# Kernel optimization log

Hardware: AMD Instinct MI355X
Metric: run time of the kernel (lower is better)

## Reference

```python
import jax, jax.numpy as jnp
import numpy as np

N, N_HUB, N_TOP = 1024, 512, 256
D_NODE, D_W, H = 128, 16, 64
E_FULL = N * (N - 1) // 2
E_HUB = N_HUB * (N_HUB - 1) // 2
E_TOP = N_TOP * (N_TOP - 1) // 2
SLOPE = 0.01  # torch F.leaky_relu default negative slope


def leaky(x):
    return jnp.where(x >= 0, x, SLOPE * x)


def gcn_conv(x, src, dst, ew, W, b, n):
    # PyG GCNConv: add self-loops (weight 1), symmetric deg^-1/2 normalization,
    # weighted sum-aggregation at destination nodes.
    loop = jnp.arange(n)
    s = jnp.concatenate([src, loop])
    d = jnp.concatenate([dst, loop])
    w = jnp.concatenate([ew, jnp.ones((n,), ew.dtype)])
    deg = jax.ops.segment_sum(w, d, num_segments=n)
    deg_safe = jnp.where(deg > 0, deg, 1.0)
    dinv = jnp.where(deg > 0, jax.lax.rsqrt(deg_safe), 0.0)
    norm = dinv[s] * w * dinv[d]          # [E + n]
    h = x @ W                              # [n, out]
    msg = h[s] * norm[:, None]             # gather + scale
    return jax.ops.segment_sum(msg, d, num_segments=n) + b


def fusion(node_attr, src, dst, edge_attr, dgW, dgb, gW, gb, cW, cb, adj_sel, edge_mask, n):
    # EdgeNodeFusion forward (dropout_rate = 0 -> dropout is identity)
    ea = leaky(edge_attr @ dgW + dgb)                       # deep-gravity Linear + LeakyReLU
    if edge_mask is not None:
        ea = ea[edge_mask]                                  # gather branch edges [E_b, H]
    sel = ea[adj_sel]                                       # directed edge attrs [E_b, H]
    s2 = jnp.concatenate([src, dst])                        # to_undirected: duplicate both ways
    d2 = jnp.concatenate([dst, src])
    w2 = jnp.concatenate([sel, sel], axis=0).mean(axis=1)   # AdaptiveAvgPool1d(1) over features
    xh = leaky(gcn_conv(node_attr, s2, d2, w2, gW, gb, n))  # [n, out]
    sim = jax.nn.sigmoid(xh @ xh.T)                         # [n, n]
    iu = jnp.triu_indices(n, k=1)
    tri = sim[iu[0], iu[1]]                                 # diag_flatten: strict upper tri, [n(n-1)/2]
    w = tri[:, None] * cW[0] + cb                           # Linear(1 -> H)
    return w * ea + ea, xh


def setup_inputs():
    key = jax.random.key(0)
    ks = jax.random.split(key, 16)
    rng = np.random.default_rng(0)

    def tri_edges(n):
        iu = np.triu_indices(n, k=1)
        return jnp.asarray(np.stack(iu).astype(np.int32))

    def lin(k, fi, fo):
        kw, kb = jax.random.split(k)
        s = 1.0 / np.sqrt(fi)
        return (jax.random.uniform(kw, (fi, fo), jnp.float32, -s, s),
                jax.random.uniform(kb, (fo,), jnp.float32, -s, s))

    inp = {}
    inp['node_hidden_z'] = jax.random.normal(ks[0], (N, D_NODE), jnp.float32)
    inp['weather_x'] = jax.random.normal(ks[1], (N, D_W), jnp.float32)
    inp['hub_weather_x'] = jax.random.normal(ks[2], (N_HUB, D_W), jnp.float32)
    inp['top_weather_x'] = jax.random.normal(ks[3], (N_TOP, D_W), jnp.float32)
    inp['edge_hidden_z'] = jax.random.normal(ks[4], (E_FULL, H), jnp.float32)
    inp['adj_index'] = tri_edges(N)
    inp['hub_adj_index'] = tri_edges(N_HUB)
    inp['top_adj_index'] = tri_edges(N_TOP)
    inp['hub_idx'] = jnp.asarray(np.sort(rng.choice(N, N_HUB, replace=False)).astype(np.int32))
    inp['top_idx'] = jnp.asarray(np.sort(rng.choice(N, N_TOP, replace=False)).astype(np.int32))
    inp['adj_sel_full'] = jnp.arange(E_FULL, dtype=jnp.int32)
    inp['adj_sel_hub'] = jnp.arange(E_HUB, dtype=jnp.int32)
    inp['adj_sel_top'] = jnp.arange(E_TOP, dtype=jnp.int32)
    inp['hub_edge_mask'] = jnp.asarray(np.sort(rng.choice(E_FULL, E_HUB, replace=False)).astype(np.int32))
    inp['top_edge_mask'] = jnp.asarray(np.sort(rng.choice(E_FULL, E_TOP, replace=False)).astype(np.int32))

    D_IN = D_NODE + D_W
    inp['dg_top_W'], inp['dg_top_b'] = lin(ks[5], H, H)
    inp['gcn_top_W'], inp['gcn_top_b'] = lin(ks[6], D_IN, D_NODE)
    inp['cat_top_W'], inp['cat_top_b'] = lin(ks[7], 1, H)
    inp['dg_hub_W'], inp['dg_hub_b'] = lin(ks[8], H, H)
    inp['gcn_hub_W'], inp['gcn_hub_b'] = lin(ks[9], D_IN, H)
    inp['cat_hub_W'], inp['cat_hub_b'] = lin(ks[10], 1, H)
    inp['dg_W'], inp['dg_b'] = lin(ks[11], H, H)
    inp['gcn_W'], inp['gcn_b'] = lin(ks[12], D_IN, H)
    inp['cat_W'], inp['cat_b'] = lin(ks[13], 1, H)
    return inp


def reference(node_hidden_z, weather_x, hub_weather_x, top_weather_x, edge_hidden_z,
              adj_index, hub_adj_index, top_adj_index, hub_idx, top_idx,
              adj_sel_full, adj_sel_hub, adj_sel_top, hub_edge_mask, top_edge_mask,
              dg_top_W, dg_top_b, gcn_top_W, gcn_top_b, cat_top_W, cat_top_b,
              dg_hub_W, dg_hub_b, gcn_hub_W, gcn_hub_b, cat_hub_W, cat_hub_b,
              dg_W, dg_b, gcn_W, gcn_b, cat_W, cat_b):
    # --- top branch ---
    top_x = jnp.concatenate([node_hidden_z[top_idx], top_weather_x], axis=-1)
    top_ea, _ = fusion(top_x, top_adj_index[0], top_adj_index[1], edge_hidden_z,
                       dg_top_W, dg_top_b, gcn_top_W, gcn_top_b, cat_top_W, cat_top_b,
                       adj_sel_top, top_edge_mask, N_TOP)
    top_full = jnp.zeros((E_FULL, H), top_ea.dtype).at[top_edge_mask].set(top_ea)  # edge_unpool
    # --- hub branch ---
    hub_x = jnp.concatenate([node_hidden_z[hub_idx], hub_weather_x], axis=-1)
    hub_ea, _ = fusion(hub_x, hub_adj_index[0], hub_adj_index[1], edge_hidden_z,
                       dg_hub_W, dg_hub_b, gcn_hub_W, gcn_hub_b, cat_hub_W, cat_hub_b,
                       adj_sel_hub, hub_edge_mask, N_HUB)
    hub_full = jnp.zeros((E_FULL, H), hub_ea.dtype).at[hub_edge_mask].set(hub_ea)  # edge_unpool
    # --- full branch ---
    x = jnp.concatenate([node_hidden_z, weather_x], axis=-1)
    full_ea, _ = fusion(x, adj_index[0], adj_index[1], edge_hidden_z,
                        dg_W, dg_b, gcn_W, gcn_b, cat_W, cat_b,
                        adj_sel_full, None, N)
    return jnp.concatenate([top_full, hub_full, full_ea], axis=-1)  # [E_FULL, 3H]


if __name__ == '__main__':
    out = reference(**setup_inputs())
    print(out.shape, out.dtype)
```

## Files before the change

kernel.cpp:

```cpp
#include <hip/hip_runtime.h>
#include <stdint.h>

#define NFULL 1024
#define NHUB  512
#define NTOP  256
#define EFULL 523776
#define EHUB  130816
#define ETOP  32640
#define ETOT  (ETOP + EHUB + EFULL)
#define NTOT  (NTOP + NHUB + NFULL)
#define HOFF_H 32768
#define HOFF_F 65536
#define HTOT   131072
#define SLOPE 0.01f

#define NB_T2 255
#define NB_H2 1022
#define NB_F2 4092

#define TT_T 10
#define TT_H 36
#define TT_F 136

__device__ __forceinline__ int trioff(int i, int n){ return (i * (2 * n - i - 1)) >> 1; }

__global__ void k_init(int* __restrict__ invT, int* __restrict__ invH)
{
  int t = blockIdx.x * 256 + threadIdx.x;
  if (t < EFULL){ invT[t] = -1; invH[t] = -1; }
}

__global__ void k_inv(const int* __restrict__ tmask, const int* __restrict__ hmask,
                      int* __restrict__ invT, int* __restrict__ invH)
{
  int t = blockIdx.x * 256 + threadIdx.x;
  if (t < ETOP) invT[tmask[t]] = t;
  else if (t < ETOP + EHUB) invH[hmask[t - ETOP]] = t - ETOP;
}

__global__ __launch_bounds__(256, 4)
void k_ea_all(const float* __restrict__ ez,
              const int* __restrict__ tmask, const int* __restrict__ hmask,
              const float* __restrict__ Wt, const float* __restrict__ bt,
              const float* __restrict__ Wh, const float* __restrict__ bh,
              const float* __restrict__ Wf, const float* __restrict__ bf,
              float* __restrict__ eat, float* __restrict__ w2_all)
{
  __shared__ float sW[4096];
  __shared__ float sB[64];
  int b = blockIdx.x, tid = threadIdx.x;
  int bloc, w2off; const int* mask; const float* W; const float* bb;
  if (b < NB_T2)               { bloc = b;                 w2off = 0;           mask = tmask;   W = Wt; bb = bt; }
  else if (b < NB_T2 + NB_H2)  { bloc = b - NB_T2;         w2off = ETOP;        mask = hmask;   W = Wh; bb = bh; }
  else                         { bloc = b - NB_T2 - NB_H2; w2off = ETOP + EHUB; mask = nullptr; W = Wf; bb = bf; }
  {
    const float4* Wv = (const float4*)W;
    float4* sWv = (float4*)sW;
    #pragma unroll
    for (int q = 0; q < 4; q++) sWv[q * 256 + tid] = Wv[q * 256 + tid];
    if (tid < 64) sB[tid] = bb[tid];
  }
  __syncthreads();
  int e_loc = bloc * 128 + (tid >> 1);
  int c0 = (tid & 1) * 32;
  int ef = mask ? mask[e_loc] : e_loc;
  const float4* row4 = (const float4*)(ez + (size_t)ef * 64);

  float acc[32];
  #pragma unroll
  for (int j = 0; j < 32; j++) acc[j] = sB[c0 + j];
  #pragma unroll
  for (int k0 = 0; k0 < 64; k0 += 4){
    float4 a4 = row4[k0 >> 2];
    float av[4]; av[0]=a4.x; av[1]=a4.y; av[2]=a4.z; av[3]=a4.w;
    #pragma unroll
    for (int q = 0; q < 4; q++){
      float a = av[q];
      const float* wr = sW + (k0 + q) * 64 + c0;
      #pragma unroll
      for (int j0 = 0; j0 < 32; j0 += 4){
        float4 w4 = *(const float4*)(wr + j0);
        acc[j0+0] += a * w4.x;
        acc[j0+1] += a * w4.y;
        acc[j0+2] += a * w4.z;
        acc[j0+3] += a * w4.w;
      }
    }
  }
  float s = 0.f;
  #pragma unroll
  for (int j = 0; j < 32; j++){
    float v = acc[j];
    v = v >= 0.f ? v : SLOPE * v;
    acc[j] = v; s += v;
  }
  s += __shfl_xor(s, 1);
  if ((tid & 1) == 0) w2_all[w2off + e_loc] = s * (1.0f / 64.0f);
  float* orow = eat + (size_t)(w2off + e_loc) * 64 + c0;
  #pragma unroll
  for (int j0 = 0; j0 < 32; j0 += 4){
    float4 o; o.x = acc[j0]; o.y = acc[j0+1]; o.z = acc[j0+2]; o.w = acc[j0+3];
    *(float4*)(orow + j0) = o;
  }
}

__global__ void k_deg_all(const float* __restrict__ w2_all, float* __restrict__ dinv_all)
{
  int b = blockIdx.x, l = threadIdx.x;
  int n, i, boff; const float* w2;
  if (b < NTOP)             { n = NTOP;  i = b;               boff = 0;           w2 = w2_all; }
  else if (b < NTOP + NHUB) { n = NHUB;  i = b - NTOP;        boff = NTOP;        w2 = w2_all + ETOP; }
  else                      { n = NFULL; i = b - NTOP - NHUB; boff = NTOP + NHUB; w2 = w2_all + ETOP + EHUB; }
  float s = 0.f;
  for (int j = l; j < n; j += 64){
    if (j == i) continue;
    int e = (j < i) ? (trioff(j, n) + i - j - 1) : (trioff(i, n) + j - i - 1);
    s += w2[e];
  }
  #pragma unroll
  for (int o = 32; o > 0; o >>= 1) s += __shfl_down(s, o);
  if (l == 0){
    float deg = s + 1.0f;
    dinv_all[boff + i] = (deg > 0.f) ? rsqrtf(deg) : 0.f;
  }
}

__global__ void k_h_all(const float* __restrict__ nodez,
                        const float* __restrict__ wx, const float* __restrict__ hwx,
                        const float* __restrict__ twx,
                        const int* __restrict__ hidx, const int* __restrict__ tidx,
                        const float* __restrict__ gWt, const float* __restrict__ gWh,
                        const float* __restrict__ gWf,
                        float* __restrict__ h_all)
{
  int t = blockIdx.x * 256 + threadIdx.x;
  if (t >= HTOT) return;
  int i, c, gout, nrow; const float* gW; const float* wxp; const int* gidx; float* hp;
  if (t < HOFF_H)      { gout = 128; i = t / 128;  c = t & 127; gW = gWt; wxp = twx; gidx = tidx; hp = h_all; }
  else if (t < HOFF_F) { int u = t - HOFF_H; gout = 64; i = u / 64; c = u & 63; gW = gWh; wxp = hwx; gidx = hidx; hp = h_all + HOFF_H; }
  else                 { int u = t - HOFF_F; gout = 64; i = u / 64; c = u & 63; gW = gWf; wxp = wx;  gidx = nullptr; hp = h_all + HOFF_F; }
  nrow = gidx ? gidx[i] : i;
  const float* nr = nodez + (size_t)nrow * 128;
  float acc = 0.f;
  for (int k = 0; k < 128; k++) acc += nr[k] * gW[k * gout + c];
  const float* wr = wxp + (size_t)i * 16;
  for (int k = 0; k < 16; k++) acc += wr[k] * gW[(128 + k) * gout + c];
  hp[(size_t)i * gout + c] = acc;
}

__global__ void k_xh_all(const float* __restrict__ w2_all, const float* __restrict__ dinv_all,
                         const float* __restrict__ h_all,
                         const float* __restrict__ gbt, const float* __restrict__ gbh,
                         const float* __restrict__ gbf,
                         float* __restrict__ xh_all)
{
  __shared__ float part[256];
  int b = blockIdx.x, tid = threadIdx.x;
  int n, i, gout; const float* w2; const float* dinv; const float* hb; const float* gb; float* xb;
  if (b < NTOP){
    n = NTOP; i = b; gout = 128;
    w2 = w2_all; dinv = dinv_all; hb = h_all; gb = gbt; xb = xh_all;
  } else if (b < NTOP + NHUB){
    n = NHUB; i = b - NTOP; gout = 64;
    w2 = w2_all + ETOP; dinv = dinv_all + NTOP; hb = h_all + HOFF_H; gb = gbh; xb = xh_all + HOFF_H;
  } else {
    n = NFULL; i = b - NTOP - NHUB; gout = 64;
    w2 = w2_all + ETOP + EHUB; dinv = dinv_all + NTOP + NHUB; hb = h_all + HOFF_F; gb = gbf; xb = xh_all + HOFF_F;
  }
  int SJ = 256 / gout;
  int c = tid & (gout - 1);
  int js = tid / gout;
  float acc = 0.f;
  for (int j = js; j < n; j += SJ){
    float coef;
    if (j == i) coef = 1.0f;
    else {
      int e = (j < i) ? (trioff(j, n) + i - j - 1) : (trioff(i, n) + j - i - 1);
      coef = w2[e];
    }
    coef *= dinv[j];
    acc += coef * hb[(size_t)j * gout + c];
  }
  part[tid] = acc;
  __syncthreads();
  if (js == 0){
    float s = acc;
    for (int q = 1; q < SJ; q++) s += part[q * gout + c];
    s = dinv[i] * s + gb[c];
    xb[(size_t)i * gout + c] = s >= 0.f ? s : SLOPE * s;
  }
}

__global__ __launch_bounds__(256)
void k_tri_tiled(const float* __restrict__ xh_all, float* __restrict__ tri_all)
{
  __shared__ float sXi[8192];
  __shared__ float sXj[8192];
  int b = blockIdx.x, tid = threadIdx.x;
  int n, g, nt, tt, csh; const float* xb; float* tb;
  if (b < TT_T)        { n = NTOP;  g = 128; nt = 4;  csh = 5; tt = b;            xb = xh_all;          tb = tri_all; }
  else if (b < TT_T+TT_H){ n = NHUB; g = 64; nt = 8;  csh = 4; tt = b - TT_T;     xb = xh_all + HOFF_H; tb = tri_all + ETOP; }
  else                 { n = NFULL; g = 64;  nt = 16; csh = 4; tt = b - TT_T - TT_H; xb = xh_all + HOFF_F; tb = tri_all + ETOP + EHUB; }
  int bi = 0, t = tt;
  while (t >= nt - bi){ t -= nt - bi; bi++; }
  int bj = bi + t;
  int cpr = g >> 2;
  int nch = 64 * cpr;
  const float* gi = xb + (size_t)(bi * 64) * g;
  const float* gj = xb + (size_t)(bj * 64) * g;
  for (int idx = tid; idx < nch; idx += 256){
    int row = idx >> csh;
    int c = idx & (cpr - 1);
    int sw = (c ^ ((row >> 2) & 7)) << 2;
    float4 v = *(const float4*)(gi + (size_t)row * g + c * 4);
    *(float4*)(sXi + row * g + sw) = v;
    float4 w = *(const float4*)(gj + (size_t)row * g + c * 4);
    *(float4*)(sXj + row * g + sw) = w;
  }
  __syncthreads();
  int ii = tid >> 4, jj = tid & 15;
  float acc[4][4];
  #pragma unroll
  for (int a = 0; a < 4; a++)
    #pragma unroll
    for (int q = 0; q < 4; q++) acc[a][q] = 0.f;
  for (int ck = 0; ck < cpr; ck++){
    int swi = (ck ^ (ii & 7)) << 2;
    int swj = (ck ^ (jj & 7)) << 2;
    float4 xi[4], xj[4];
    #pragma unroll
    for (int a = 0; a < 4; a++) xi[a] = *(const float4*)(sXi + (ii * 4 + a) * g + swi);
    #pragma unroll
    for (int q = 0; q < 4; q++) xj[q] = *(const float4*)(sXj + (jj * 4 + q) * g + swj);
    #pragma unroll
    for (int a = 0; a < 4; a++)
      #pragma unroll
      for (int q = 0; q < 4; q++){
        acc[a][q] += xi[a].x * xj[q].x;
        acc[a][q] += xi[a].y * xj[q].y;
        acc[a][q] += xi[a].z * xj[q].z;
        acc[a][q] += xi[a].w * xj[q].w;
      }
  }
  #pragma unroll
  for (int a = 0; a < 4; a++){
    int I = bi * 64 + ii * 4 + a;
    int base = trioff(I, n) - I - 1;
    #pragma unroll
    for (int q = 0; q < 4; q++){
      int J = bj * 64 + jj * 4 + q;
      if (I < J){
        float s = acc[a][q];
        tb[base + J] = 1.f / (1.f + __expf(-s));
      }
    }
  }
}

__global__ void k_final(const float* __restrict__ eat, const float* __restrict__ tri_all,
                        const int* __restrict__ invT, const int* __restrict__ invH,
                        const float* __restrict__ cwT, const float* __restrict__ cbT,
                        const float* __restrict__ cwH, const float* __restrict__ cbH,
                        const float* __restrict__ cwF, const float* __restrict__ cbF,
                        float* __restrict__ out)
{
  __shared__ float cw[3][64], cb[3][64];
  int lt = threadIdx.x;
  if (lt < 64)       { cw[0][lt] = cwT[lt]; cb[0][lt] = cbT[lt]; }
  else if (lt < 128) { int l = lt - 64;  cw[1][l] = cwH[l]; cb[1][l] = cbH[l]; }
  else if (lt < 192) { int l = lt - 128; cw[2][l] = cwF[l]; cb[2][l] = cbF[l]; }
  __syncthreads();
  int t = blockIdx.x * 256 + threadIdx.x;
  const int TOT = EFULL * 48;
  if (t >= TOT) return;
  int e = t / 48;
  int c = t - e * 48;
  int br = c >> 4, h0 = (c & 15) * 4;
  int eb, ebase; const float* tri;
  if (br == 0)      { eb = invT[e]; tri = tri_all;               ebase = 0; }
  else if (br == 1) { eb = invH[e]; tri = tri_all + ETOP;        ebase = ETOP; }
  else              { eb = e;       tri = tri_all + ETOP + EHUB; ebase = ETOP + EHUB; }
  float* p = out + (size_t)e * 192 + br * 64 + h0;
  if (eb >= 0){
    float tv = tri[eb];
    const float* q = eat + (size_t)(ebase + eb) * 64 + h0;
    float4 v = *(const float4*)q;
    float4 o;
    o.x = v.x * (1.f + tv * cw[br][h0+0] + cb[br][h0+0]);
    o.y = v.y * (1.f + tv * cw[br][h0+1] + cb[br][h0+1]);
    o.z = v.z * (1.f + tv * cw[br][h0+2] + cb[br][h0+2]);
    o.w = v.w * (1.f + tv * cw[br][h0+3] + cb[br][h0+3]);
    *(float4*)p = o;
  } else {
    float4 z; z.x = 0.f; z.y = 0.f; z.z = 0.f; z.w = 0.f;
    *(float4*)p = z;
  }
}

extern "C" void kernel_launch(void* const* d_in, const int* in_sizes, int n_in,
                              void* d_out, int out_size, void* d_ws, size_t ws_size,
                              hipStream_t stream)
{
  const float* nodez  = (const float*)d_in[0];
  const float* wx     = (const float*)d_in[1];
  const float* hub_wx = (const float*)d_in[2];
  const float* top_wx = (const float*)d_in[3];
  const float* ez     = (const float*)d_in[4];
  const int* hidx  = (const int*)d_in[8];
  const int* tidx  = (const int*)d_in[9];
  const int* hmask = (const int*)d_in[13];
  const int* tmask = (const int*)d_in[14];
  const float* dgW_t = (const float*)d_in[15];
  const float* dgb_t = (const float*)d_in[16];
  const float* gW_t  = (const float*)d_in[17];
  const float* gb_t  = (const float*)d_in[18];
  const float* cW_t  = (const float*)d_in[19];
  const float* cb_t  = (const float*)d_in[20];
  const float* dgW_h = (const float*)d_in[21];
  const float* dgb_h = (const float*)d_in[22];
  const float* gW_h  = (const float*)d_in[23];
  const float* gb_h  = (const float*)d_in[24];
  const float* cW_h  = (const float*)d_in[25];
  const float* cb_h  = (const float*)d_in[26];
  const float* dgW_f = (const float*)d_in[27];
  const float* dgb_f = (const float*)d_in[28];
  const float* gW_f  = (const float*)d_in[29];
  const float* gb_f  = (const float*)d_in[30];
  const float* cW_f  = (const float*)d_in[31];
  const float* cb_f  = (const float*)d_in[32];

  char* w = (char*)d_ws;
  size_t off = 0;
  auto alloc = [&](size_t bytes) -> char* {
    char* p = w + off;
    off += (bytes + 255) & ~(size_t)255;
    return p;
  };
  float* w2_all   = (float*)alloc((size_t)ETOT * 4);
  float* tri_all  = (float*)alloc((size_t)ETOT * 4);
  float* dinv_all = (float*)alloc((size_t)NTOT * 4);
  float* h_all    = (float*)alloc((size_t)HTOT * 4);
  float* xh_all   = (float*)alloc((size_t)HTOT * 4);
  int* invT       = (int*)alloc((size_t)EFULL * 4);
  int* invH       = (int*)alloc((size_t)EFULL * 4);
  float* eat      = (float*)alloc((size_t)ETOT * 64 * 4);
  (void)ws_size; (void)in_sizes; (void)n_in; (void)out_size;

  float* outp = (float*)d_out;

  k_init<<<(EFULL + 255) / 256, 256, 0, stream>>>(invT, invH);
  k_inv<<<(ETOP + EHUB + 255) / 256, 256, 0, stream>>>(tmask, hmask, invT, invH);
  k_ea_all<<<NB_T2 + NB_H2 + NB_F2, 256, 0, stream>>>(ez, tmask, hmask,
      dgW_t, dgb_t, dgW_h, dgb_h, dgW_f, dgb_f, eat, w2_all);
  k_h_all<<<(HTOT + 255) / 256, 256, 0, stream>>>(nodez, wx, hub_wx, top_wx,
      hidx, tidx, gW_t, gW_h, gW_f, h_all);
  k_deg_all<<<NTOT, 64, 0, stream>>>(w2_all, dinv_all);
  k_xh_all<<<NTOT, 256, 0, stream>>>(w2_all, dinv_all, h_all, gb_t, gb_h, gb_f, xh_all);
  k_tri_tiled<<<TT_T + TT_H + TT_F, 256, 0, stream>>>(xh_all, tri_all);
  k_final<<<(EFULL * 48 + 255) / 256, 256, 0, stream>>>(
      eat, tri_all, invT, invH, cW_t, cb_t, cW_h, cb_h, cW_f, cb_f, outp);
}
```

Baseline: 862.3 us.

## Register-tile edge Linear in k_ea_all with swizzled LDS staging of inputs

```diff
diff --git a/kernel.cpp b/kernel.cpp
--- a/kernel.cpp
+++ b/kernel.cpp
@@ -14,9 +14,9 @@
 #define HTOT   131072
 #define SLOPE 0.01f
 
-#define NB_T2 255
-#define NB_H2 1022
-#define NB_F2 4092
+#define NB_T3 128
+#define NB_H3 511
+#define NB_F3 2046
 
 #define TT_T 10
 #define TT_H 36
@@ -38,7 +38,7 @@
   else if (t < ETOP + EHUB) invH[hmask[t - ETOP]] = t - ETOP;
 }
 
-__global__ __launch_bounds__(256, 4)
+__global__ __launch_bounds__(256, 2)
 void k_ea_all(const float* __restrict__ ez,
               const int* __restrict__ tmask, const int* __restrict__ hmask,
               const float* __restrict__ Wt, const float* __restrict__ bt,
@@ -47,60 +47,101 @@
               float* __restrict__ eat, float* __restrict__ w2_all)
 {
   __shared__ float sW[4096];
-  __shared__ float sB[64];
+  __shared__ float sA[16384];
   int b = blockIdx.x, tid = threadIdx.x;
-  int bloc, w2off; const int* mask; const float* W; const float* bb;
-  if (b < NB_T2)               { bloc = b;                 w2off = 0;           mask = tmask;   W = Wt; bb = bt; }
-  else if (b < NB_T2 + NB_H2)  { bloc = b - NB_T2;         w2off = ETOP;        mask = hmask;   W = Wh; bb = bh; }
-  else                         { bloc = b - NB_T2 - NB_H2; w2off = ETOP + EHUB; mask = nullptr; W = Wf; bb = bf; }
+  int bloc, w2off, E; const int* mask; const float* W; const float* bb;
+  if (b < NB_T3)               { bloc = b;                 E = ETOP;  w2off = 0;           mask = tmask;   W = Wt; bb = bt; }
+  else if (b < NB_T3 + NB_H3)  { bloc = b - NB_T3;         E = EHUB;  w2off = ETOP;        mask = hmask;   W = Wh; bb = bh; }
+  else                         { bloc = b - NB_T3 - NB_H3; E = EFULL; w2off = ETOP + EHUB; mask = nullptr; W = Wf; bb = bf; }
+  int e0 = bloc * 256;
   {
     const float4* Wv = (const float4*)W;
     float4* sWv = (float4*)sW;
     #pragma unroll
     for (int q = 0; q < 4; q++) sWv[q * 256 + tid] = Wv[q * 256 + tid];
-    if (tid < 64) sB[tid] = bb[tid];
+  }
+  #pragma unroll
+  for (int it = 0; it < 16; it++){
+    int idx = it * 256 + tid;
+    int row = idx >> 4, ch = idx & 15;
+    int er = e0 + row;
+    int ec = er < E ? er : (E - 1);
+    int ef = mask ? mask[ec] : ec;
+    float4 v = *(const float4*)(ez + (size_t)ef * 64 + ch * 4);
+    int sch = ch ^ ((row >> 3) & 7);
+    *(float4*)(sA + row * 64 + sch * 4) = v;
   }
   __syncthreads();
-  int e_loc = bloc * 128 + (tid >> 1);
-  int c0 = (tid & 1) * 32;
-  int ef = mask ? mask[e_loc] : e_loc;
-  const float4* row4 = (const float4*)(ez + (size_t)ef * 64);
-
-  float acc[32];
-  #pragma unroll
-  for (int j = 0; j < 32; j++) acc[j] = sB[c0 + j];
-  #pragma unroll
-  for (int k0 = 0; k0 < 64; k0 += 4){
-    float4 a4 = row4[k0 >> 2];
-    float av[4]; av[0]=a4.x; av[1]=a4.y; av[2]=a4.z; av[3]=a4.w;
+
+  int g = tid >> 3, c8 = tid & 7;
+  int rbase = g * 8;
+  int swz = (g & 7) << 2;
+  const float* wbase = sW + c8 * 8;
+
+  float bias[8];
+  #pragma unroll
+  for (int j = 0; j < 8; j++) bias[j] = bb[c8 * 8 + j];
+  float acc[8][8];
+  #pragma unroll
+  for (int e = 0; e < 8; e++)
+    #pragma unroll
+    for (int j = 0; j < 8; j++) acc[e][j] = bias[j];
+
+  #pragma unroll
+  for (int ch = 0; ch < 16; ch++){
+    int sa_off = (ch << 2) ^ swz;
+    float4 a[8];
+    #pragma unroll
+    for (int e = 0; e < 8; e++) a[e] = *(const float4*)(sA + (rbase + e) * 64 + sa_off);
     #pragma unroll
     for (int q = 0; q < 4; q++){
-      float a = av[q];
-      const float* wr = sW + (k0 + q) * 64 + c0;
+      const float* wr = wbase + (ch * 4 + q) * 64;
+      float4 w0 = *(const float4*)(wr);
+      float4 w1 = *(const float4*)(wr + 4);
+      float wv[8]; wv[0]=w0.x; wv[1]=w0.y; wv[2]=w0.z; wv[3]=w0.w;
+      wv[4]=w1.x; wv[5]=w1.y; wv[6]=w1.z; wv[7]=w1.w;
       #pragma unroll
-      for (int j0 = 0; j0 < 32; j0 += 4){
-        float4 w4 = *(const float4*)(wr + j0);
-        acc[j0+0] += a * w4.x;
-        acc[j0+1] += a * w4.y;
-        acc[j0+2] += a * w4.z;
-        acc[j0+3] += a * w4.w;
+      for (int e = 0; e < 8; e++){
+        float av = (q == 0) ? a[e].x : (q == 1) ? a[e].y : (q == 2) ? a[e].z : a[e].w;
+        #pragma unroll
+        for (int j = 0; j < 8; j++) acc[e][j] += av * wv[j];
       }
     }
   }
-  float s = 0.f;
-  #pragma unroll
-  for (int j = 0; j < 32; j++){
-    float v = acc[j];
-    v = v >= 0.f ? v : SLOPE * v;
-    acc[j] = v; s += v;
-  }
-  s += __shfl_xor(s, 1);
-  if ((tid & 1) == 0) w2_all[w2off + e_loc] = s * (1.0f / 64.0f);
-  float* orow = eat + (size_t)(w2off + e_loc) * 64 + c0;
-  #pragma unroll
-  for (int j0 = 0; j0 < 32; j0 += 4){
-    float4 o; o.x = acc[j0]; o.y = acc[j0+1]; o.z = acc[j0+2]; o.w = acc[j0+3];
-    *(float4*)(orow + j0) = o;
+
+  float psum[8];
+  #pragma unroll
+  for (int e = 0; e < 8; e++){
+    float s = 0.f;
+    #pragma unroll
+    for (int j = 0; j < 8; j++){
+      float v = acc[e][j];
+      v = v >= 0.f ? v : SLOPE * v;
+      acc[e][j] = v; s += v;
+    }
+    psum[e] = s;
+  }
+  #pragma unroll
+  for (int o = 1; o < 8; o <<= 1)
+    #pragma unroll
+    for (int e = 0; e < 8; e++) psum[e] += __shfl_xor(psum[e], o);
+  if (c8 == 0){
+    #pragma unroll
+    for (int e = 0; e < 8; e++){
+      int er = e0 + rbase + e;
+      if (er < E) w2_all[w2off + er] = psum[e] * (1.0f / 64.0f);
+    }
+  }
+  #pragma unroll
+  for (int e = 0; e < 8; e++){
+    int er = e0 + rbase + e;
+    if (er < E){
+      float* orow = eat + (size_t)(w2off + er) * 64 + c8 * 8;
+      float4 o0; o0.x = acc[e][0]; o0.y = acc[e][1]; o0.z = acc[e][2]; o0.w = acc[e][3];
+      float4 o1; o1.x = acc[e][4]; o1.y = acc[e][5]; o1.z = acc[e][6]; o1.w = acc[e][7];
+      *(float4*)(orow) = o0;
+      *(float4*)(orow + 4) = o1;
+    }
   }
 }
 
@@ -350,7 +391,7 @@
 
   k_init<<<(EFULL + 255) / 256, 256, 0, stream>>>(invT, invH);
   k_inv<<<(ETOP + EHUB + 255) / 256, 256, 0, stream>>>(tmask, hmask, invT, invH);
-  k_ea_all<<<NB_T2 + NB_H2 + NB_F2, 256, 0, stream>>>(ez, tmask, hmask,
+  k_ea_all<<<NB_T3 + NB_H3 + NB_F3, 256, 0, stream>>>(ez, tmask, hmask,
       dgW_t, dgb_t, dgW_h, dgb_h, dgW_f, dgb_f, eat, w2_all);
   k_h_all<<<(HTOT + 255) / 256, 256, 0, stream>>>(nodez, wx, hub_wx, top_wx,
       hidx, tidx, gW_t, gW_h, gW_f, h_all);
```

After: 882.7 us. +2.4%, slower.

## Replace inverse-mask gather with zero-fill plus branch scatter; cache GCN coefficients

Applied to the files above, without the earlier changes.

```diff
diff --git a/kernel.cpp b/kernel.cpp
--- a/kernel.cpp
+++ b/kernel.cpp
@@ -22,20 +22,20 @@
 #define TT_H 36
 #define TT_F 136
 
+#define NBZ  65472
+#define NBT4 2040
+#define NBH4 8176
+#define NBF4 32736
+
 __device__ __forceinline__ int trioff(int i, int n){ return (i * (2 * n - i - 1)) >> 1; }
 
-__global__ void k_init(int* __restrict__ invT, int* __restrict__ invH)
+__global__ __launch_bounds__(256)
+void k_zero(float* __restrict__ out)
 {
   int t = blockIdx.x * 256 + threadIdx.x;
-  if (t < EFULL){ invT[t] = -1; invH[t] = -1; }
-}
-
-__global__ void k_inv(const int* __restrict__ tmask, const int* __restrict__ hmask,
-                      int* __restrict__ invT, int* __restrict__ invH)
-{
-  int t = blockIdx.x * 256 + threadIdx.x;
-  if (t < ETOP) invT[tmask[t]] = t;
-  else if (t < ETOP + EHUB) invH[hmask[t - ETOP]] = t - ETOP;
+  int row = t >> 5, c4 = t & 31;
+  float4 z; z.x = 0.f; z.y = 0.f; z.z = 0.f; z.w = 0.f;
+  *(float4*)(out + (size_t)row * 192 + c4 * 4) = z;
 }
 
 __global__ __launch_bounds__(256, 4)
@@ -106,21 +106,24 @@
 
 __global__ void k_deg_all(const float* __restrict__ w2_all, float* __restrict__ dinv_all)
 {
+  __shared__ float red[4];
   int b = blockIdx.x, l = threadIdx.x;
   int n, i, boff; const float* w2;
   if (b < NTOP)             { n = NTOP;  i = b;               boff = 0;           w2 = w2_all; }
   else if (b < NTOP + NHUB) { n = NHUB;  i = b - NTOP;        boff = NTOP;        w2 = w2_all + ETOP; }
   else                      { n = NFULL; i = b - NTOP - NHUB; boff = NTOP + NHUB; w2 = w2_all + ETOP + EHUB; }
   float s = 0.f;
-  for (int j = l; j < n; j += 64){
+  for (int j = l; j < n; j += 256){
     if (j == i) continue;
     int e = (j < i) ? (trioff(j, n) + i - j - 1) : (trioff(i, n) + j - i - 1);
     s += w2[e];
   }
   #pragma unroll
   for (int o = 32; o > 0; o >>= 1) s += __shfl_down(s, o);
+  if ((l & 63) == 0) red[l >> 6] = s;
+  __syncthreads();
   if (l == 0){
-    float deg = s + 1.0f;
+    float deg = red[0] + red[1] + red[2] + red[3] + 1.0f;
     dinv_all[boff + i] = (deg > 0.f) ? rsqrtf(deg) : 0.f;
   }
 }
@@ -154,6 +157,7 @@
                          const float* __restrict__ gbf,
                          float* __restrict__ xh_all)
 {
+  __shared__ float coef[1024];
   __shared__ float part[256];
   int b = blockIdx.x, tid = threadIdx.x;
   int n, i, gout; const float* w2; const float* dinv; const float* hb; const float* gb; float* xb;
@@ -167,19 +171,23 @@
     n = NFULL; i = b - NTOP - NHUB; gout = 64;
     w2 = w2_all + ETOP + EHUB; dinv = dinv_all + NTOP + NHUB; hb = h_all + HOFF_F; gb = gbf; xb = xh_all + HOFF_F;
   }
+  for (int j = tid; j < n; j += 256){
+    float w;
+    if (j == i) w = 1.0f;
+    else {
+      int e = (j < i) ? (trioff(j, n) + i - j - 1) : (trioff(i, n) + j - i - 1);
+      w = w2[e];
+    }
+    coef[j] = w * dinv[j];
+  }
+  __syncthreads();
   int SJ = 256 / gout;
   int c = tid & (gout - 1);
   int js = tid / gout;
   float acc = 0.f;
+  #pragma unroll 4
   for (int j = js; j < n; j += SJ){
-    float coef;
-    if (j == i) coef = 1.0f;
-    else {
-      int e = (j < i) ? (trioff(j, n) + i - j - 1) : (trioff(i, n) + j - i - 1);
-      coef = w2[e];
-    }
-    coef *= dinv[j];
-    acc += coef * hb[(size_t)j * gout + c];
+    acc += coef[j] * hb[(size_t)j * gout + c];
   }
   part[tid] = acc;
   __syncthreads();
@@ -257,44 +265,34 @@
   }
 }
 
-__global__ void k_final(const float* __restrict__ eat, const float* __restrict__ tri_all,
-                        const int* __restrict__ invT, const int* __restrict__ invH,
-                        const float* __restrict__ cwT, const float* __restrict__ cbT,
-                        const float* __restrict__ cwH, const float* __restrict__ cbH,
-                        const float* __restrict__ cwF, const float* __restrict__ cbF,
-                        float* __restrict__ out)
-{
-  __shared__ float cw[3][64], cb[3][64];
-  int lt = threadIdx.x;
-  if (lt < 64)       { cw[0][lt] = cwT[lt]; cb[0][lt] = cbT[lt]; }
-  else if (lt < 128) { int l = lt - 64;  cw[1][l] = cwH[l]; cb[1][l] = cbH[l]; }
-  else if (lt < 192) { int l = lt - 128; cw[2][l] = cwF[l]; cb[2][l] = cbF[l]; }
-  __syncthreads();
-  int t = blockIdx.x * 256 + threadIdx.x;
-  const int TOT = EFULL * 48;
-  if (t >= TOT) return;
-  int e = t / 48;
-  int c = t - e * 48;
-  int br = c >> 4, h0 = (c & 15) * 4;
-  int eb, ebase; const float* tri;
-  if (br == 0)      { eb = invT[e]; tri = tri_all;               ebase = 0; }
-  else if (br == 1) { eb = invH[e]; tri = tri_all + ETOP;        ebase = ETOP; }
-  else              { eb = e;       tri = tri_all + ETOP + EHUB; ebase = ETOP + EHUB; }
-  float* p = out + (size_t)e * 192 + br * 64 + h0;
-  if (eb >= 0){
-    float tv = tri[eb];
-    const float* q = eat + (size_t)(ebase + eb) * 64 + h0;
-    float4 v = *(const float4*)q;
-    float4 o;
-    o.x = v.x * (1.f + tv * cw[br][h0+0] + cb[br][h0+0]);
-    o.y = v.y * (1.f + tv * cw[br][h0+1] + cb[br][h0+1]);
-    o.z = v.z * (1.f + tv * cw[br][h0+2] + cb[br][h0+2]);
-    o.w = v.w * (1.f + tv * cw[br][h0+3] + cb[br][h0+3]);
-    *(float4*)p = o;
-  } else {
-    float4 z; z.x = 0.f; z.y = 0.f; z.z = 0.f; z.w = 0.f;
-    *(float4*)p = z;
-  }
+__global__ __launch_bounds__(256)
+void k_out(const float* __restrict__ eat, const float* __restrict__ tri_all,
+           const int* __restrict__ tmask, const int* __restrict__ hmask,
+           const float* __restrict__ cwT, const float* __restrict__ cbT,
+           const float* __restrict__ cwH, const float* __restrict__ cbH,
+           const float* __restrict__ cwF, const float* __restrict__ cbF,
+           float* __restrict__ out)
+{
+  __shared__ float scw[64], scb[64];
+  int b = blockIdx.x, tid = threadIdx.x;
+  int boff, col, u; const int* mask; const float* cwp; const float* cbp;
+  if (b < NBT4)             { u = b * 256 + tid;                 boff = 0;           col = 0;   mask = tmask;   cwp = cwT; cbp = cbT; }
+  else if (b < NBT4 + NBH4) { u = (b - NBT4) * 256 + tid;        boff = ETOP;        col = 64;  mask = hmask;   cwp = cwH; cbp = cbH; }
+  else                      { u = (b - NBT4 - NBH4) * 256 + tid; boff = ETOP + EHUB; col = 128; mask = nullptr; cwp = cwF; cbp = cbF; }
+  if (tid < 64){ scw[tid] = cwp[tid]; scb[tid] = cbp[tid]; }
+  __syncthreads();
+  int eb = u >> 4, c4 = u & 15;
+  int erow = mask ? mask[eb] : eb;
+  float tv = tri_all[boff + eb];
+  const float* q = eat + (size_t)(boff + eb) * 64 + c4 * 4;
+  float4 v = *(const float4*)q;
+  int h0 = c4 * 4;
+  float4 o;
+  o.x = v.x * (1.f + tv * scw[h0+0] + scb[h0+0]);
+  o.y = v.y * (1.f + tv * scw[h0+1] + scb[h0+1]);
+  o.z = v.z * (1.f + tv * scw[h0+2] + scb[h0+2]);
+  o.w = v.w * (1.f + tv * scw[h0+3] + scb[h0+3]);
+  *(float4*)(out + (size_t)erow * 192 + col + h0) = o;
 }
 
 extern "C" void kernel_launch(void* const* d_in, const int* in_sizes, int n_in,
@@ -341,22 +339,19 @@
   float* dinv_all = (float*)alloc((size_t)NTOT * 4);
   float* h_all    = (float*)alloc((size_t)HTOT * 4);
   float* xh_all   = (float*)alloc((size_t)HTOT * 4);
-  int* invT       = (int*)alloc((size_t)EFULL * 4);
-  int* invH       = (int*)alloc((size_t)EFULL * 4);
   float* eat      = (float*)alloc((size_t)ETOT * 64 * 4);
   (void)ws_size; (void)in_sizes; (void)n_in; (void)out_size;
 
   float* outp = (float*)d_out;
 
-  k_init<<<(EFULL + 255) / 256, 256, 0, stream>>>(invT, invH);
-  k_inv<<<(ETOP + EHUB + 255) / 256, 256, 0, stream>>>(tmask, hmask, invT, invH);
+  k_zero<<<NBZ, 256, 0, stream>>>(outp);
   k_ea_all<<<NB_T2 + NB_H2 + NB_F2, 256, 0, stream>>>(ez, tmask, hmask,
       dgW_t, dgb_t, dgW_h, dgb_h, dgW_f, dgb_f, eat, w2_all);
   k_h_all<<<(HTOT + 255) / 256, 256, 0, stream>>>(nodez, wx, hub_wx, top_wx,
       hidx, tidx, gW_t, gW_h, gW_f, h_all);
-  k_deg_all<<<NTOT, 64, 0, stream>>>(w2_all, dinv_all);
+  k_deg_all<<<NTOT, 256, 0, stream>>>(w2_all, dinv_all);
   k_xh_all<<<NTOT, 256, 0, stream>>>(w2_all, dinv_all, h_all, gb_t, gb_h, gb_f, xh_all);
   k_tri_tiled<<<TT_T + TT_H + TT_F, 256, 0, stream>>>(xh_all, tri_all);
-  k_final<<<(EFULL * 48 + 255) / 256, 256, 0, stream>>>(
-      eat, tri_all, invT, invH, cW_t, cb_t, cW_h, cb_h, cW_f, cb_f, outp);
-}
+  k_out<<<NBT4 + NBH4 + NBF4, 256, 0, stream>>>(
+      eat, tri_all, tmask, hmask, cW_t, cb_t, cW_h, cb_h, cW_f, cb_f, outp);
+}
```

New measurement: 733.9 us. 14.9% less time.
